# Performance work log

Measured on AMD Instinct MI355X. Metric: run time of the kernel, lower is better.

Reference implementation:

```python
import jax, jax.numpy as jnp
import numpy as np

# Geometry constants matching PointLoss.__init__ defaults
FOV_H = 360.0   # horizontal FOV (deg)
FOV_VU = 3.0    # upper vertical FOV (deg)
DH = 0.5        # delta_h
DV = 0.5        # delta_v
PROJ_H = 52     # int(26 / 0.5)
PROJ_W = 720    # int(360 / 0.5)
THETAC = 0.5    # confidence threshold
LAMDA = 1.0     # fov-loss weight
ANGRATE = 1.0   # anglelossrate
EPS = 1e-8


def setup_inputs() -> dict:
    key = jax.random.key(0)
    ks = jax.random.split(key, 10)
    B, H, W = 64, PROJ_H, PROJ_W
    return {
        "vertexmap_proj": jax.random.normal(ks[0], (B, H, W, 3), jnp.float32),
        "normalmap_proj": jax.random.normal(ks[1], (B, H, W, 3), jnp.float32),
        "uncertainty": jax.random.uniform(ks[2], (B, H, W), jnp.float32),
        "now_normalmap": jax.random.normal(ks[3], (B, H, W, 3), jnp.float32),
        "now_confidencemap": jax.random.uniform(ks[4], (B, H, W), jnp.float32),
        "last_normalmap": jax.random.normal(ks[5], (B, H, W, 3), jnp.float32),
        "last_vertexmap": jax.random.normal(ks[6], (B, H, W, 3), jnp.float32),
        "sx": jnp.zeros((1,), jnp.float32),
        "sq": jnp.zeros((1,), jnp.float32),
        "now_maskmap": jax.random.randint(ks[7], (B, H, W), 0, 2, jnp.int32),
        "last_maskmap": jax.random.randint(ks[8], (B, H, W), 0, 2, jnp.int32),
    }


def _gather_proj(m, flat_idx, B, H, W):
    """Gather pixels of m [B,H,W,(C)] at flat index [B,H,W] -> same shape as m."""
    if m.ndim == 3:
        mf = m.reshape(B, H * W)
        return jnp.take_along_axis(mf, flat_idx.reshape(B, H * W), axis=1).reshape(B, H, W)
    C = m.shape[-1]
    mf = m.reshape(B, H * W, C)
    idx = jnp.broadcast_to(flat_idx.reshape(B, H * W, 1), (B, H * W, C))
    return jnp.take_along_axis(mf, idx, axis=1).reshape(B, H, W, C)


def reference(vertexmap_proj, normalmap_proj, uncertainty, now_normalmap,
              now_confidencemap, last_normalmap, last_vertexmap, sx, sq,
              now_maskmap, last_maskmap):
    B, H, W, _ = vertexmap_proj.shape
    v = vertexmap_proj

    # mask of valid current pixels: maskmap > 0 and normal non-zero
    mask0 = (now_maskmap > 0) & (jnp.sum(jnp.abs(now_normalmap), -1) != 0)

    # spherical re-projection (movegrid=True)
    depth = jnp.sqrt(jnp.sum(v * v, -1) + EPS)
    yaw = jnp.arctan2(v[..., 1], v[..., 0]) * (180.0 / np.pi)
    pitch = jnp.arcsin(jnp.clip(v[..., 2] / depth, -1.0, 1.0)) * (180.0 / np.pi)
    proj_x = (FOV_H / 2 - yaw) / DH
    proj_y = (FOV_VU - pitch) / DV

    # fov loss = masked mse(proj, clamp(proj)) (F.mse_loss default mean)
    m0 = mask0.astype(v.dtype)
    n0 = jnp.maximum(jnp.sum(m0), 1.0)
    fovloss = (jnp.sum(m0 * (proj_x - jnp.clip(proj_x, 0, W - 1)) ** 2)
               + jnp.sum(m0 * (proj_y - jnp.clip(proj_y, 0, H - 1)) ** 2)) / n0

    prx = jnp.round(proj_x)
    pry = jnp.round(proj_y)
    inb = (prx >= 0) & (prx < W) & (pry >= 0) & (pry < H)
    prxi = jnp.clip(prx, 0, W - 1).astype(jnp.int32)
    pryi = jnp.clip(pry, 0, H - 1).astype(jnp.int32)
    flat = pryi * W + prxi  # [B,H,W]

    nl = _gather_proj(last_normalmap, flat, B, H, W)   # last normal at projected pixel
    vl = _gather_proj(last_vertexmap, flat, B, H, W)   # last vertex at projected pixel
    lm = _gather_proj(last_maskmap, flat, B, H, W)

    lastmask = (lm > 0) & (jnp.sum(jnp.abs(nl), -1) != 0)
    mask = mask0 & inb & lastmask & (now_confidencemap >= THETAC)
    m = mask.astype(v.dtype)
    n = jnp.maximum(jnp.sum(m), 1.0)

    # point-to-plane ICP residual, uncertainty-weighted L1
    r = jnp.sum(nl * (v - vl), -1)
    icploss = jnp.sum(m * uncertainty * jnp.abs(r)) / n

    # angular loss: 1 - |cos(angle between normals)|
    nn = normalmap_proj
    cosang = jnp.abs(jnp.sum(nl * nn, -1)) / jnp.sqrt(
        jnp.sum(nl * nl, -1) * jnp.sum(nn * nn, -1) + EPS)
    angloss = jnp.sum(m * uncertainty * (1.0 - cosang)) / n

    sx0, sq0 = sx[0], sq[0]
    total = (jnp.exp(-sx0) * icploss + sx0
             + ANGRATE * jnp.exp(-sq0) * angloss + sq0
             + LAMDA * fovloss)
    return total
```

## Files before the change

kernel.cpp:

```cpp
#include <hip/hip_runtime.h>
#include <math.h>


namespace {
constexpr int B_ = 64, H_ = 52, W_ = 720;
constexpr int HW_ = H_ * W_;
constexpr int NPIX = B_ * HW_;
constexpr int NTHREADS = 256;
constexpr int NBLOCKS = 2048;
constexpr int STRIDE = NBLOCKS * NTHREADS;
constexpr int NITER = (NPIX + STRIDE - 1) / STRIDE;
constexpr float EPSF = 1e-8f;
constexpr float RAD2DEG = 57.29577951308232f;
}

__global__ __launch_bounds__(NTHREADS) void pointloss_main(
    const float* __restrict__ v,
    const float* __restrict__ nrm,
    const float* __restrict__ unc,
    const float* __restrict__ nown,
    const float* __restrict__ conf,
    const float* __restrict__ lastn,
    const float* __restrict__ lastv,
    const int*   __restrict__ nowm,
    const int*   __restrict__ lastm,
    float* __restrict__ partials)
{
    float s_m0 = 0.f, s_fov = 0.f, s_m = 0.f, s_icp = 0.f, s_ang = 0.f;

    int p = blockIdx.x * NTHREADS + threadIdx.x;

    float vx = v[3*p+0],  vy = v[3*p+1],  vz = v[3*p+2];
    float ax = nown[3*p+0], ay = nown[3*p+1], az = nown[3*p+2];
    int   mi = nowm[p];
    float cfv = conf[p];
    float uv  = unc[p];

    #pragma unroll
    for (int it = 0; it < NITER; ++it) {
        const int pn = p + STRIDE;
        const bool hasnext = (it + 1 < NITER) && (pn < NPIX);
        const int pl = hasnext ? pn : p;
        const float nvx = v[3*pl+0],  nvy = v[3*pl+1],  nvz = v[3*pl+2];
        const float nax = nown[3*pl+0], nay = nown[3*pl+1], naz = nown[3*pl+2];
        const int   nmi = nowm[pl];
        const float ncf = conf[pl];
        const float nuv = unc[pl];

        const bool valid = (p < NPIX);
        const bool mask0 = valid && (mi > 0) &&
                           ((fabsf(ax) + fabsf(ay) + fabsf(az)) != 0.0f);

        const float d2 = vx*vx + vy*vy + vz*vz + EPSF;
        const float depth = sqrtf(d2);
        const float yaw   = atan2f(vy, vx) * RAD2DEG;
        const float q     = fminf(fmaxf(vz / depth, -1.f), 1.f);
        const float pitch = asinf(q) * RAD2DEG;
        const float px = (180.0f - yaw) * 2.0f;
        const float py = (3.0f - pitch) * 2.0f;

        if (mask0) {
            const float dx = px - fminf(fmaxf(px, 0.f), (float)(W_ - 1));
            const float dy = py - fminf(fmaxf(py, 0.f), (float)(H_ - 1));
            s_m0 += 1.0f;
            s_fov += dx*dx + dy*dy;
        }

        const float prx = rintf(px), pry = rintf(py);
        const bool inb = (prx >= 0.f) && (prx < (float)W_) &&
                         (pry >= 0.f) && (pry < (float)H_);

        if (mask0 && inb && (cfv >= 0.5f)) {
            const int gi = (p / HW_) * HW_ + (int)pry * W_ + (int)prx;
            const float lx = lastn[3*gi+0], ly = lastn[3*gi+1], lz = lastn[3*gi+2];
            const int   lmv = lastm[gi];
            const float wx = lastv[3*gi+0], wy = lastv[3*gi+1], wz = lastv[3*gi+2];
            const float nx = nrm[3*p+0],   ny = nrm[3*p+1],   nz = nrm[3*p+2];
            if ((lmv > 0) && ((fabsf(lx) + fabsf(ly) + fabsf(lz)) != 0.f)) {
                const float r  = lx*(vx-wx) + ly*(vy-wy) + lz*(vz-wz);
                const float dt = lx*nx + ly*ny + lz*nz;
                const float den = (lx*lx + ly*ly + lz*lz) *
                                  (nx*nx + ny*ny + nz*nz) + EPSF;
                const float cosang = fabsf(dt) * rsqrtf(den);
                s_m   += 1.0f;
                s_icp += uv * fabsf(r);
                s_ang += uv * (1.0f - cosang);
            }
        }

        vx = nvx; vy = nvy; vz = nvz;
        ax = nax; ay = nay; az = naz;
        mi = nmi; cfv = ncf; uv = nuv;
        p = pn;
    }

    #pragma unroll
    for (int off = 32; off > 0; off >>= 1) {
        s_m0  += __shfl_down(s_m0,  off);
        s_fov += __shfl_down(s_fov, off);
        s_m   += __shfl_down(s_m,   off);
        s_icp += __shfl_down(s_icp, off);
        s_ang += __shfl_down(s_ang, off);
    }
    __shared__ float red[NTHREADS / 64][5];
    const int lane = threadIdx.x & 63;
    const int wv   = threadIdx.x >> 6;
    if (lane == 0) {
        red[wv][0] = s_m0;  red[wv][1] = s_fov; red[wv][2] = s_m;
        red[wv][3] = s_icp; red[wv][4] = s_ang;
    }
    __syncthreads();
    if (threadIdx.x == 0) {
        float tt[5] = {0.f, 0.f, 0.f, 0.f, 0.f};
        for (int w2 = 0; w2 < NTHREADS / 64; ++w2)
            for (int c = 0; c < 5; ++c) tt[c] += red[w2][c];
        float* o = partials + blockIdx.x * 5;
        for (int c = 0; c < 5; ++c) o[c] = tt[c];
    }
}

__global__ __launch_bounds__(256) void pointloss_finalize(
    const float* __restrict__ partials,
    const float* __restrict__ sx,
    const float* __restrict__ sq,
    float* __restrict__ out)
{
    double a0 = 0, a1 = 0, a2 = 0, a3 = 0, a4 = 0;
    for (int i = threadIdx.x; i < NBLOCKS; i += 256) {
        const float* pp = partials + i * 5;
        a0 += (double)pp[0]; a1 += (double)pp[1]; a2 += (double)pp[2];
        a3 += (double)pp[3]; a4 += (double)pp[4];
    }
    #pragma unroll
    for (int off = 32; off > 0; off >>= 1) {
        a0 += __shfl_down(a0, off);
        a1 += __shfl_down(a1, off);
        a2 += __shfl_down(a2, off);
        a3 += __shfl_down(a3, off);
        a4 += __shfl_down(a4, off);
    }
    __shared__ double red[4][5];
    const int lane = threadIdx.x & 63;
    const int wv   = threadIdx.x >> 6;
    if (lane == 0) {
        red[wv][0] = a0; red[wv][1] = a1; red[wv][2] = a2;
        red[wv][3] = a3; red[wv][4] = a4;
    }
    __syncthreads();
    if (threadIdx.x == 0) {
        double t[5] = {0, 0, 0, 0, 0};
        for (int w2 = 0; w2 < 4; ++w2)
            for (int c = 0; c < 5; ++c) t[c] += red[w2][c];
        const double n0 = fmax(t[0], 1.0);
        const double n  = fmax(t[2], 1.0);
        const double sx0 = (double)sx[0], sq0 = (double)sq[0];
        const double total = exp(-sx0) * (t[3] / n) + sx0
                           + exp(-sq0) * (t[4] / n) + sq0
                           + t[1] / n0;
        out[0] = (float)total;
    }
}

extern "C" void kernel_launch(void* const* d_in, const int* in_sizes, int n_in,
                              void* d_out, int out_size, void* d_ws, size_t ws_size,
                              hipStream_t stream) {
    const float* v     = (const float*)d_in[0];
    const float* nrm   = (const float*)d_in[1];
    const float* unc   = (const float*)d_in[2];
    const float* nown  = (const float*)d_in[3];
    const float* conf  = (const float*)d_in[4];
    const float* lastn = (const float*)d_in[5];
    const float* lastv = (const float*)d_in[6];
    const float* sx    = (const float*)d_in[7];
    const float* sq    = (const float*)d_in[8];
    const int*   nowm  = (const int*)d_in[9];
    const int*   lastm = (const int*)d_in[10];

    float* partials = (float*)d_ws;

    pointloss_main<<<NBLOCKS, NTHREADS, 0, stream>>>(
        v, nrm, unc, nown, conf, lastn, lastv, nowm, lastm, partials);
    pointloss_finalize<<<1, 256, 0, stream>>>(partials, sx, sq, (float*)d_out);
}
```

Measured before the change: 194.5 us.

## Compact valid pixels into a queue and gather in a separate phase

```diff
diff --git a/kernel.cpp b/kernel.cpp
--- a/kernel.cpp
+++ b/kernel.cpp
@@ -6,150 +6,238 @@
 constexpr int B_ = 64, H_ = 52, W_ = 720;
 constexpr int HW_ = H_ * W_;
 constexpr int NPIX = B_ * HW_;
-constexpr int NTHREADS = 256;
-constexpr int NBLOCKS = 2048;
-constexpr int STRIDE = NBLOCKS * NTHREADS;
+constexpr int NT = 256;
+constexpr int NB1 = 2048;
+constexpr int STRIDE = NB1 * NT;
 constexpr int NITER = (NPIX + STRIDE - 1) / STRIDE;
+constexpr int NB2 = 256;
 constexpr float EPSF = 1e-8f;
 constexpr float RAD2DEG = 57.29577951308232f;
-}
-
-__global__ __launch_bounds__(NTHREADS) void pointloss_main(
+constexpr size_t OFF_CNT = 0;
+constexpr size_t OFF_P1  = 256;
+constexpr size_t OFF_P2  = OFF_P1 + (size_t)NB1 * 2 * 4;
+constexpr size_t OFF_Q   = 65536;
+}
+
+__device__ __forceinline__ float atan_poly01(float z) {
+    const float z2 = z * z;
+    float r = fmaf(z2, -0.0117212f, 0.0526526f);
+    r = fmaf(z2, r, -0.1164329f);
+    r = fmaf(z2, r,  0.1935435f);
+    r = fmaf(z2, r, -0.3326235f);
+    r = fmaf(z2, r,  0.9999773f);
+    return r * z;
+}
+
+__device__ __forceinline__ float atan2_fast(float y, float x) {
+    const float ax = fabsf(x), ay = fabsf(y);
+    const float mx = fmaxf(ax, ay), mn = fminf(ax, ay);
+    const float z = mn * __builtin_amdgcn_rcpf(fmaxf(mx, 1e-37f));
+    float a = atan_poly01(z);
+    if (ay > ax) a = 1.5707964f - a;
+    if (x < 0.0f) a = 3.1415927f - a;
+    return copysignf(a, y);
+}
+
+__device__ __forceinline__ float asin_core(float x) {
+    const float x2 = x * x;
+    float r = fmaf(x2, 0.03038196f, 0.04464286f);
+    r = fmaf(x2, r, 0.075f);
+    r = fmaf(x2, r, 0.16666667f);
+    return fmaf(x * x2, r, x);
+}
+
+__device__ __forceinline__ float asin_fast(float q) {
+    const float a = fabsf(q);
+    const float r1 = asin_core(a);
+    const float s = sqrtf(fmaxf(0.5f * (1.0f - a), 0.0f));
+    const float r2 = 1.5707964f - 2.0f * asin_core(s);
+    const float r = (a > 0.5f) ? r2 : r1;
+    return copysignf(r, q);
+}
+
+__global__ __launch_bounds__(NT) void pl_phase1(
     const float* __restrict__ v,
-    const float* __restrict__ nrm,
-    const float* __restrict__ unc,
     const float* __restrict__ nown,
     const float* __restrict__ conf,
-    const float* __restrict__ lastn,
-    const float* __restrict__ lastv,
     const int*   __restrict__ nowm,
-    const int*   __restrict__ lastm,
-    float* __restrict__ partials)
+    unsigned int* __restrict__ counter,
+    int2* __restrict__ queue, unsigned int cap,
+    float* __restrict__ p1)
 {
-    float s_m0 = 0.f, s_fov = 0.f, s_m = 0.f, s_icp = 0.f, s_ang = 0.f;
-
-    int p = blockIdx.x * NTHREADS + threadIdx.x;
-
-    float vx = v[3*p+0],  vy = v[3*p+1],  vz = v[3*p+2];
-    float ax = nown[3*p+0], ay = nown[3*p+1], az = nown[3*p+2];
+    float s_m0 = 0.f, s_fov = 0.f;
+    const int lane = threadIdx.x & 63;
+    int p = blockIdx.x * NT + threadIdx.x;
+
+    float vx = v[3*p], vy = v[3*p+1], vz = v[3*p+2];
+    float ax = nown[3*p], ay = nown[3*p+1], az = nown[3*p+2];
     int   mi = nowm[p];
-    float cfv = conf[p];
-    float uv  = unc[p];
+    float cf = conf[p];
 
     #pragma unroll
     for (int it = 0; it < NITER; ++it) {
         const int pn = p + STRIDE;
         const bool hasnext = (it + 1 < NITER) && (pn < NPIX);
         const int pl = hasnext ? pn : p;
-        const float nvx = v[3*pl+0],  nvy = v[3*pl+1],  nvz = v[3*pl+2];
-        const float nax = nown[3*pl+0], nay = nown[3*pl+1], naz = nown[3*pl+2];
+        const float nvx = v[3*pl], nvy = v[3*pl+1], nvz = v[3*pl+2];
+        const float nax = nown[3*pl], nay = nown[3*pl+1], naz = nown[3*pl+2];
         const int   nmi = nowm[pl];
         const float ncf = conf[pl];
-        const float nuv = unc[pl];
 
         const bool valid = (p < NPIX);
         const bool mask0 = valid && (mi > 0) &&
                            ((fabsf(ax) + fabsf(ay) + fabsf(az)) != 0.0f);
 
         const float d2 = vx*vx + vy*vy + vz*vz + EPSF;
-        const float depth = sqrtf(d2);
-        const float yaw   = atan2f(vy, vx) * RAD2DEG;
-        const float q     = fminf(fmaxf(vz / depth, -1.f), 1.f);
-        const float pitch = asinf(q) * RAD2DEG;
+        const float q  = fminf(fmaxf(vz * __builtin_amdgcn_rsqf(d2), -1.f), 1.f);
+        const float yaw   = atan2_fast(vy, vx) * RAD2DEG;
+        const float pitch = asin_fast(q) * RAD2DEG;
         const float px = (180.0f - yaw) * 2.0f;
         const float py = (3.0f - pitch) * 2.0f;
 
         if (mask0) {
-            const float dx = px - fminf(fmaxf(px, 0.f), (float)(W_ - 1));
-            const float dy = py - fminf(fmaxf(py, 0.f), (float)(H_ - 1));
+            const float dx = px - fminf(fmaxf(px, 0.f), 719.0f);
+            const float dy = py - fminf(fmaxf(py, 0.f), 51.0f);
             s_m0 += 1.0f;
             s_fov += dx*dx + dy*dy;
         }
 
         const float prx = rintf(px), pry = rintf(py);
-        const bool inb = (prx >= 0.f) && (prx < (float)W_) &&
-                         (pry >= 0.f) && (pry < (float)H_);
-
-        if (mask0 && inb && (cfv >= 0.5f)) {
-            const int gi = (p / HW_) * HW_ + (int)pry * W_ + (int)prx;
-            const float lx = lastn[3*gi+0], ly = lastn[3*gi+1], lz = lastn[3*gi+2];
-            const int   lmv = lastm[gi];
-            const float wx = lastv[3*gi+0], wy = lastv[3*gi+1], wz = lastv[3*gi+2];
-            const float nx = nrm[3*p+0],   ny = nrm[3*p+1],   nz = nrm[3*p+2];
-            if ((lmv > 0) && ((fabsf(lx) + fabsf(ly) + fabsf(lz)) != 0.f)) {
-                const float r  = lx*(vx-wx) + ly*(vy-wy) + lz*(vz-wz);
-                const float dt = lx*nx + ly*ny + lz*nz;
-                const float den = (lx*lx + ly*ly + lz*lz) *
-                                  (nx*nx + ny*ny + nz*nz) + EPSF;
-                const float cosang = fabsf(dt) * rsqrtf(den);
-                s_m   += 1.0f;
-                s_icp += uv * fabsf(r);
-                s_ang += uv * (1.0f - cosang);
+        const bool inb = (prx >= 0.f) && (prx < 720.f) &&
+                         (pry >= 0.f) && (pry < 52.f);
+        const bool pred = mask0 && inb && (cf >= 0.5f);
+
+        const unsigned long long bal = __ballot(pred);
+        if (bal) {
+            unsigned int base = 0;
+            if (lane == 0) base = atomicAdd(counter, (unsigned)__popcll(bal));
+            base = (unsigned)__shfl((int)base, 0);
+            if (pred) {
+                const unsigned int idx =
+                    base + (unsigned)__popcll(bal & ((1ull << lane) - 1ull));
+                if (idx < cap) {
+                    const int gi = (p / HW_) * HW_ + (int)pry * W_ + (int)prx;
+                    queue[idx] = make_int2(p, gi);
+                }
             }
         }
 
         vx = nvx; vy = nvy; vz = nvz;
         ax = nax; ay = nay; az = naz;
-        mi = nmi; cfv = ncf; uv = nuv;
-        p = pn;
+        mi = nmi; cf = ncf; p = pn;
     }
 
     #pragma unroll
     for (int off = 32; off > 0; off >>= 1) {
         s_m0  += __shfl_down(s_m0,  off);
         s_fov += __shfl_down(s_fov, off);
+    }
+    __shared__ float red[NT / 64][2];
+    const int wv = threadIdx.x >> 6;
+    if (lane == 0) { red[wv][0] = s_m0; red[wv][1] = s_fov; }
+    __syncthreads();
+    if (threadIdx.x == 0) {
+        float a = 0.f, b = 0.f;
+        for (int w2 = 0; w2 < NT / 64; ++w2) { a += red[w2][0]; b += red[w2][1]; }
+        p1[blockIdx.x * 2 + 0] = a;
+        p1[blockIdx.x * 2 + 1] = b;
+    }
+}
+
+__global__ __launch_bounds__(NT) void pl_phase2(
+    const float* __restrict__ v,
+    const float* __restrict__ nrm,
+    const float* __restrict__ unc,
+    const float* __restrict__ lastn,
+    const float* __restrict__ lastv,
+    const int*   __restrict__ lastm,
+    const unsigned int* __restrict__ counter,
+    const int2* __restrict__ queue, unsigned int cap,
+    float* __restrict__ p2)
+{
+    float s_m = 0.f, s_icp = 0.f, s_ang = 0.f;
+    unsigned int count = *counter;
+    if (count > cap) count = cap;
+    const unsigned int gsz = NB2 * NT;
+    for (unsigned int i = blockIdx.x * NT + threadIdx.x; i < count; i += gsz) {
+        const int2 rec = queue[i];
+        const int p = rec.x, gi = rec.y;
+        const float lx = lastn[3*gi], ly = lastn[3*gi+1], lz = lastn[3*gi+2];
+        const int   lmv = lastm[gi];
+        const float wx = lastv[3*gi], wy = lastv[3*gi+1], wz = lastv[3*gi+2];
+        const float nx = nrm[3*p],  ny = nrm[3*p+1],  nz = nrm[3*p+2];
+        const float u  = unc[p];
+        const float vx = v[3*p], vy = v[3*p+1], vz = v[3*p+2];
+        if ((lmv > 0) && ((fabsf(lx) + fabsf(ly) + fabsf(lz)) != 0.f)) {
+            const float r  = lx*(vx-wx) + ly*(vy-wy) + lz*(vz-wz);
+            const float dt = lx*nx + ly*ny + lz*nz;
+            const float den = (lx*lx + ly*ly + lz*lz) *
+                              (nx*nx + ny*ny + nz*nz) + EPSF;
+            const float cosang = fabsf(dt) * __builtin_amdgcn_rsqf(den);
+            s_m   += 1.0f;
+            s_icp += u * fabsf(r);
+            s_ang += u * (1.0f - cosang);
+        }
+    }
+
+    #pragma unroll
+    for (int off = 32; off > 0; off >>= 1) {
         s_m   += __shfl_down(s_m,   off);
         s_icp += __shfl_down(s_icp, off);
         s_ang += __shfl_down(s_ang, off);
     }
-    __shared__ float red[NTHREADS / 64][5];
+    __shared__ float red[NT / 64][3];
     const int lane = threadIdx.x & 63;
-    const int wv   = threadIdx.x >> 6;
-    if (lane == 0) {
-        red[wv][0] = s_m0;  red[wv][1] = s_fov; red[wv][2] = s_m;
-        red[wv][3] = s_icp; red[wv][4] = s_ang;
-    }
+    const int wv = threadIdx.x >> 6;
+    if (lane == 0) { red[wv][0] = s_m; red[wv][1] = s_icp; red[wv][2] = s_ang; }
     __syncthreads();
     if (threadIdx.x == 0) {
-        float tt[5] = {0.f, 0.f, 0.f, 0.f, 0.f};
-        for (int w2 = 0; w2 < NTHREADS / 64; ++w2)
-            for (int c = 0; c < 5; ++c) tt[c] += red[w2][c];
-        float* o = partials + blockIdx.x * 5;
-        for (int c = 0; c < 5; ++c) o[c] = tt[c];
-    }
-}
-
-__global__ __launch_bounds__(256) void pointloss_finalize(
-    const float* __restrict__ partials,
+        float a = 0.f, b = 0.f, c = 0.f;
+        for (int w2 = 0; w2 < NT / 64; ++w2) {
+            a += red[w2][0]; b += red[w2][1]; c += red[w2][2];
+        }
+        p2[blockIdx.x * 3 + 0] = a;
+        p2[blockIdx.x * 3 + 1] = b;
+        p2[blockIdx.x * 3 + 2] = c;
+    }
+}
+
+__global__ __launch_bounds__(NT) void pl_finalize(
+    const float* __restrict__ p1,
+    const float* __restrict__ p2,
     const float* __restrict__ sx,
     const float* __restrict__ sq,
     float* __restrict__ out)
 {
-    double a0 = 0, a1 = 0, a2 = 0, a3 = 0, a4 = 0;
-    for (int i = threadIdx.x; i < NBLOCKS; i += 256) {
-        const float* pp = partials + i * 5;
-        a0 += (double)pp[0]; a1 += (double)pp[1]; a2 += (double)pp[2];
-        a3 += (double)pp[3]; a4 += (double)pp[4];
+    double m0 = 0, fov = 0, m = 0, icp = 0, ang = 0;
+    for (int i = threadIdx.x; i < NB1; i += NT) {
+        m0  += (double)p1[i*2+0];
+        fov += (double)p1[i*2+1];
+    }
+    if (threadIdx.x < NB2) {
+        m   += (double)p2[threadIdx.x*3+0];
+        icp += (double)p2[threadIdx.x*3+1];
+        ang += (double)p2[threadIdx.x*3+2];
     }
     #pragma unroll
     for (int off = 32; off > 0; off >>= 1) {
-        a0 += __shfl_down(a0, off);
-        a1 += __shfl_down(a1, off);
-        a2 += __shfl_down(a2, off);
-        a3 += __shfl_down(a3, off);
-        a4 += __shfl_down(a4, off);
-    }
-    __shared__ double red[4][5];
+        m0  += __shfl_down(m0,  off);
+        fov += __shfl_down(fov, off);
+        m   += __shfl_down(m,   off);
+        icp += __shfl_down(icp, off);
+        ang += __shfl_down(ang, off);
+    }
+    __shared__ double red[NT / 64][5];
     const int lane = threadIdx.x & 63;
-    const int wv   = threadIdx.x >> 6;
+    const int wv = threadIdx.x >> 6;
     if (lane == 0) {
-        red[wv][0] = a0; red[wv][1] = a1; red[wv][2] = a2;
-        red[wv][3] = a3; red[wv][4] = a4;
+        red[wv][0] = m0; red[wv][1] = fov; red[wv][2] = m;
+        red[wv][3] = icp; red[wv][4] = ang;
     }
     __syncthreads();
     if (threadIdx.x == 0) {
         double t[5] = {0, 0, 0, 0, 0};
-        for (int w2 = 0; w2 < 4; ++w2)
+        for (int w2 = 0; w2 < NT / 64; ++w2)
             for (int c = 0; c < 5; ++c) t[c] += red[w2][c];
         const double n0 = fmax(t[0], 1.0);
         const double n  = fmax(t[2], 1.0);
@@ -176,9 +264,19 @@
     const int*   nowm  = (const int*)d_in[9];
     const int*   lastm = (const int*)d_in[10];
 
-    float* partials = (float*)d_ws;
-
-    pointloss_main<<<NBLOCKS, NTHREADS, 0, stream>>>(
-        v, nrm, unc, nown, conf, lastn, lastv, nowm, lastm, partials);
-    pointloss_finalize<<<1, 256, 0, stream>>>(partials, sx, sq, (float*)d_out);
-}
+    char* ws = (char*)d_ws;
+    unsigned int* counter = (unsigned int*)(ws + OFF_CNT);
+    float* p1 = (float*)(ws + OFF_P1);
+    float* p2 = (float*)(ws + OFF_P2);
+    int2*  queue = (int2*)(ws + OFF_Q);
+    size_t qcap = (ws_size > OFF_Q + sizeof(int2))
+                      ? (ws_size - OFF_Q) / sizeof(int2) : 0;
+    if (qcap > (size_t)NPIX) qcap = NPIX;
+    const unsigned int cap = (unsigned int)qcap;
+
+    hipMemsetAsync(counter, 0, sizeof(unsigned int), stream);
+    pl_phase1<<<NB1, NT, 0, stream>>>(v, nown, conf, nowm, counter, queue, cap, p1);
+    pl_phase2<<<NB2, NT, 0, stream>>>(v, nrm, unc, lastn, lastv, lastm,
+                                      counter, queue, cap, p2);
+    pl_finalize<<<1, NT, 0, stream>>>(p1, p2, sx, sq, (float*)d_out);
+}
```

Result: slower. 591.0 us (+203.8%).
